# Optimization experiments

Hardware: AMD Instinct MI355X
Metric: run time of the kernel (lower is better)

The kernel has to match this reference:

```python
import jax, jax.numpy as jnp
import numpy as np

NUM_BINS = 64
Z_MIN, Z_MAX = -3.0, 1.0
BIN_SIZE = (Z_MAX - Z_MIN) / NUM_BINS
EPS_MEAN = 1e-5
EPS_BN = 1e-5


def setup_inputs() -> dict:
    key = jax.random.key(0)
    k1, k2, k3, k4 = jax.random.split(key, 4)
    M, N, C = 100000, 64, 4
    feat_channels, out_dim = 64, NUM_BINS * 3
    features = jax.random.normal(k1, (M, N, C), dtype=jnp.float32)
    num_points = jax.random.randint(k2, (M,), 0, 65, dtype=jnp.int32)
    coors = jax.random.randint(k3, (M, 4), 0, 100, dtype=jnp.int32)
    W = jax.random.normal(k4, (feat_channels, out_dim), dtype=jnp.float32) * (1.0 / np.sqrt(out_dim))
    b = jnp.zeros((feat_channels,), dtype=jnp.float32)
    gamma = jnp.ones((feat_channels,), dtype=jnp.float32)
    beta = jnp.zeros((feat_channels,), dtype=jnp.float32)
    return {"features": features, "num_points": num_points, "coors": coors,
            "W": W, "b": b, "gamma": gamma, "beta": beta}


def reference(features, num_points, coors, W, b, gamma, beta):
    M, N, C = features.shape
    # validity mask per point
    mask = (jnp.arange(N)[None, :] < num_points[:, None]).astype(features.dtype)  # [M, N]
    z = features[..., 2]  # [M, N]
    r = features[..., 3]  # [M, N]
    bin_idx = jnp.clip(((z - Z_MIN) / BIN_SIZE).astype(jnp.int32), 0, NUM_BINS - 1)  # [M, N]

    rows = jnp.arange(M)[:, None]  # [M, 1] broadcast against [M, N]
    zeros = jnp.zeros((M, NUM_BINS), dtype=features.dtype)
    count = zeros.at[rows, bin_idx].add(mask)
    sum_z = zeros.at[rows, bin_idx].add(z * mask)
    sum_r = zeros.at[rows, bin_idx].add(r * mask)
    mean_z = sum_z / (count + EPS_MEAN)
    mean_r = sum_r / (count + EPS_MEAN)

    # interleaved layout [count, mean_z, mean_r] per bin -> [M, 3*NUM_BINS]
    hist = jnp.stack([count, mean_z, mean_r], axis=-1).reshape(M, NUM_BINS * 3)

    # Linear -> BatchNorm1d (training: biased batch stats) -> ReLU
    x = hist @ W.T + b  # [M, feat_channels]
    mu = jnp.mean(x, axis=0)
    var = jnp.mean((x - mu) ** 2, axis=0)
    xn = (x - mu) / jnp.sqrt(var + EPS_BN)
    return jax.nn.relu(xn * gamma + beta)
```

## Files before the change

kernel.cpp:

```cpp
#include <hip/hip_runtime.h>
#include <hip/hip_bf16.h>
#include <math.h>


typedef __attribute__((ext_vector_type(8))) short bf16x8;
typedef __attribute__((ext_vector_type(4))) float f32x4;
typedef __attribute__((ext_vector_type(4))) int   i32x4;

#define ZMINF   (-3.0f)
#define INV_BIN 16.0f
#define HROWS   16
#define HPAD    196
#define SZF     524288.0f
#define INV_SZF (1.0f / 524288.0f)
#define TSC     16777216.0f
#define INV_TSC (1.0f / 16777216.0f)
#define REPS    16

__device__ __forceinline__ short f2bf(float f) {
    __hip_bfloat16 h = __float2bfloat16(f);
    return __builtin_bit_cast(short, h);
}

__global__ __launch_bounds__(256)
void k0_prep(const float* __restrict__ W,
             short*       __restrict__ wsW,
             unsigned long long* __restrict__ totals)
{
    const int tid = threadIdx.x;
    for (int e = tid; e < 24 * 64 * 8; e += 256) {
        const int j  = e & 7;
        const int ln = (e >> 3) & 63;
        const int st = e >> 9;
        const int s  = st >> 2, t = st & 3;
        const int k  = s * 32 + (ln >> 4) * 8 + j;
        const int n  = t * 16 + (ln & 15);
        const int wc = (k < 64) ? 3 * k
                     : (k < 128) ? 3 * (k - 64) + 1
                                 : 3 * (k - 128) + 2;
        wsW[e] = f2bf(W[n * 192 + wc]);
    }
    for (int e = tid; e < REPS * 128; e += 256) totals[e] = 0ull;
}

__global__ __launch_bounds__(256, 3)
void k1_hist_mfma(const float4* __restrict__ feat,
                  const int*    __restrict__ nump,
                  const bf16x8* __restrict__ wsWf,
                  const float*  __restrict__ bvec,
                  float*        __restrict__ xout,
                  unsigned long long* __restrict__ totals,
                  int M)
{
    __shared__ int sH[4 * HROWS * HPAD];

    const int tid  = threadIdx.x;
    const int wave = tid >> 6;
    const int lane = tid & 63;
    const int col  = lane & 15;
    const int quad = lane >> 4;

    const int gbase = (blockIdx.x * 4 + wave) * HROWS;
    int* hw = &sH[wave * HROWS * HPAD];
    float psum[4] = {0.f, 0.f, 0.f, 0.f};
    float psq[4]  = {0.f, 0.f, 0.f, 0.f};

    if (gbase < M) {
        i32x4* p4 = (i32x4*)hw;
        #pragma unroll
        for (int i = 0; i < 13; ++i) {
            const int idx = lane + i * 64;
            if (idx < (HROWS * HPAD) / 4) p4[idx] = i32x4{0, 0, 0, 0};
        }
        __builtin_amdgcn_wave_barrier();

        float4 v[HROWS]; int np[HROWS];
        #pragma unroll
        for (int u = 0; u < HROWS; ++u) {
            const int row = gbase + u;
            const int rc  = min(row, M - 1);
            v[u]  = feat[(size_t)rc * 64 + lane];
            np[u] = (row < M) ? nump[rc] : 0;
        }
        #pragma unroll
        for (int u = 0; u < HROWS; ++u) {
            if (lane < np[u]) {
                const float z = v[u].z, rr = v[u].w;
                int bi = (int)((z - ZMINF) * INV_BIN);
                bi = min(max(bi, 0), 63);
                int* hrow = hw + u * HPAD;
                atomicAdd(hrow + bi, 1);
                atomicAdd(hrow + 64 + bi, (int)(z * SZF));
                atomicAdd(hrow + 128 + bi, (int)(rr * SZF));
            }
        }
        __builtin_amdgcn_wave_barrier();
        __threadfence_block();

        f32x4 acc[4] = {};
        bf16x8 bcur[4], bnxt[4];
        #pragma unroll
        for (int t = 0; t < 4; ++t) bcur[t] = wsWf[t * 64 + lane];

        const int* ar = hw + col * HPAD + quad * 8;
        float c0[8], c1[8];
        #pragma unroll
        for (int s = 0; s < 6; ++s) {
            if (s < 5) {
                #pragma unroll
                for (int t = 0; t < 4; ++t) bnxt[t] = wsWf[((s + 1) * 4 + t) * 64 + lane];
            }
            const i32x4* ap = (const i32x4*)(ar + s * 32);
            const i32x4 a0 = ap[0], a1 = ap[1];
            const int iv[8] = {a0.x, a0.y, a0.z, a0.w, a1.x, a1.y, a1.z, a1.w};
            float av[8];
            if (s == 0) {
                #pragma unroll
                for (int j = 0; j < 8; ++j) { c0[j] = (float)iv[j]; av[j] = c0[j]; }
            } else if (s == 1) {
                #pragma unroll
                for (int j = 0; j < 8; ++j) { c1[j] = (float)iv[j]; av[j] = c1[j]; }
            } else if (s == 2) {
                #pragma unroll
                for (int j = 0; j < 8; ++j) {
                    c0[j] = __builtin_amdgcn_rcpf(c0[j] + 1e-5f) * INV_SZF;
                    av[j] = (float)iv[j] * c0[j];
                }
            } else if (s == 3) {
                #pragma unroll
                for (int j = 0; j < 8; ++j) {
                    c1[j] = __builtin_amdgcn_rcpf(c1[j] + 1e-5f) * INV_SZF;
                    av[j] = (float)iv[j] * c1[j];
                }
            } else if (s == 4) {
                #pragma unroll
                for (int j = 0; j < 8; ++j) av[j] = (float)iv[j] * c0[j];
            } else {
                #pragma unroll
                for (int j = 0; j < 8; ++j) av[j] = (float)iv[j] * c1[j];
            }
            bf16x8 af;
            #pragma unroll
            for (int j = 0; j < 8; ++j) af[j] = f2bf(av[j]);
            #pragma unroll
            for (int t = 0; t < 4; ++t)
                acc[t] = __builtin_amdgcn_mfma_f32_16x16x32_bf16(af, bcur[t], acc[t], 0, 0, 0);
            #pragma unroll
            for (int t = 0; t < 4; ++t) bcur[t] = bnxt[t];
        }

        #pragma unroll
        for (int t = 0; t < 4; ++t) {
            const float bias = bvec[t * 16 + col];
            #pragma unroll
            for (int i = 0; i < 4; ++i) {
                const int row = gbase + quad * 4 + i;
                if (row < M) {
                    const float xv = acc[t][i] + bias;
                    xout[(size_t)row * 64 + t * 16 + col] = xv;
                    psum[t] += xv;
                    psq[t]  += xv * xv;
                }
            }
        }
    }

    #pragma unroll
    for (int t = 0; t < 4; ++t) {
        psum[t] += __shfl_xor(psum[t], 16);
        psum[t] += __shfl_xor(psum[t], 32);
        psq[t]  += __shfl_xor(psq[t], 16);
        psq[t]  += __shfl_xor(psq[t], 32);
    }
    __syncthreads();
    float* sF = (float*)sH;
    float* hw2 = sF + wave * HROWS * HPAD;
    if (quad == 0) {
        #pragma unroll
        for (int t = 0; t < 4; ++t) {
            hw2[t * 16 + col]      = psum[t];
            hw2[64 + t * 16 + col] = psq[t];
        }
    }
    __syncthreads();
    if (tid < 128) {
        const float tot = sF[tid] + sF[HROWS * HPAD + tid]
                        + sF[2 * HROWS * HPAD + tid] + sF[3 * HROWS * HPAD + tid];
        unsigned long long* dst = totals + (blockIdx.x & (REPS - 1)) * 128 + tid;
        atomicAdd(dst, (unsigned long long)(long long)(tot * TSC));
    }
}

__global__ __launch_bounds__(256)
void k3_bn_apply(float4* __restrict__ x,
                 const unsigned long long* __restrict__ totals,
                 const float* __restrict__ gamma,
                 const float* __restrict__ beta,
                 float invM, int n4)
{
    __shared__ float sT[128];
    __shared__ float sa[64];
    __shared__ float sc[64];
    const int t = threadIdx.x;
    if (t < 128) {
        long long s = 0;
        #pragma unroll
        for (int rep = 0; rep < REPS; ++rep) s += (long long)totals[rep * 128 + t];
        sT[t] = (float)s * (invM * INV_TSC);
    }
    __syncthreads();
    if (t < 64) {
        const float mu   = sT[t];
        const float q    = sT[64 + t];
        const float var  = q - mu * mu;
        const float rstd = 1.0f / sqrtf(var + 1e-5f);
        const float a    = gamma[t] * rstd;
        sa[t] = a;
        sc[t] = beta[t] - mu * a;
    }
    __syncthreads();
    const int i = blockIdx.x * 256 + t;
    if (i >= n4) return;
    const float4 a = ((const float4*)sa)[i & 15];
    const float4 c = ((const float4*)sc)[i & 15];
    float4 v = x[i];
    v.x = fmaxf(fmaf(v.x, a.x, c.x), 0.f);
    v.y = fmaxf(fmaf(v.y, a.y, c.y), 0.f);
    v.z = fmaxf(fmaf(v.z, a.z, c.z), 0.f);
    v.w = fmaxf(fmaf(v.w, a.w, c.w), 0.f);
    x[i] = v;
}

extern "C" void kernel_launch(void* const* d_in, const int* in_sizes, int n_in,
                              void* d_out, int out_size, void* d_ws, size_t ws_size,
                              hipStream_t stream) {
    const float4* feat  = (const float4*)d_in[0];
    const int*    nump  = (const int*)d_in[1];
    const float*  W     = (const float*)d_in[3];
    const float*  bvec  = (const float*)d_in[4];
    const float*  gamma = (const float*)d_in[5];
    const float*  beta  = (const float*)d_in[6];

    const int M = in_sizes[1];
    float* xout = (float*)d_out;
    short* wsW  = (short*)d_ws;
    unsigned long long* totals =
        (unsigned long long*)((char*)d_ws + 24 * 64 * 8 * sizeof(short));

    k0_prep<<<1, 256, 0, stream>>>(W, wsW, totals);

    const int nblk = (M + 4 * HROWS - 1) / (4 * HROWS);
    k1_hist_mfma<<<nblk, 256, 0, stream>>>(feat, nump, (const bf16x8*)wsW, bvec, xout, totals, M);

    const int n4 = out_size / 4;
    k3_bn_apply<<<(n4 + 255) / 256, 256, 0, stream>>>((float4*)d_out, totals, gamma, beta,
                                                      1.0f / (float)M, n4);
}
```

Measured before the change: 206.1 us.

## Make histogram kernel persistent with prefetching and load only z/r halves

The histogram+MFMA kernel becomes a persistent grid of 512 blocks whose waves loop over row groups, prefetching the next group's features while the current one is processed. Only the z and r components are loaded, as uint2, and the per-row point counts come from one per-lane load followed by readlane. The block-level LDS reduction of BN statistics is replaced by per-wave atomics into 64 replica slots. The BN apply kernel becomes grid-stride with 16 float4 per thread. These trade occupancy-based latency hiding for explicit software prefetch and add more global atomics per block.

Result: slower. 231.6 us (+12.3%).

```diff
diff --git a/kernel.cpp b/kernel.cpp
--- a/kernel.cpp
+++ b/kernel.cpp
@@ -15,7 +15,9 @@
 #define INV_SZF (1.0f / 524288.0f)
 #define TSC     16777216.0f
 #define INV_TSC (1.0f / 16777216.0f)
-#define REPS    16
+#define REPS    64
+#define NBLK1   512
+#define NWAVES  (NBLK1 * 4)
 
 __device__ __forceinline__ short f2bf(float f) {
     __hip_bfloat16 h = __float2bfloat16(f);
@@ -44,13 +46,13 @@
 }
 
 __global__ __launch_bounds__(256, 3)
-void k1_hist_mfma(const float4* __restrict__ feat,
+void k1_hist_mfma(const uint2*  __restrict__ feat2,
                   const int*    __restrict__ nump,
                   const bf16x8* __restrict__ wsWf,
                   const float*  __restrict__ bvec,
                   float*        __restrict__ xout,
                   unsigned long long* __restrict__ totals,
-                  int M)
+                  int M, int G)
 {
     __shared__ int sH[4 * HROWS * HPAD];
 
@@ -59,33 +61,47 @@
     const int lane = tid & 63;
     const int col  = lane & 15;
     const int quad = lane >> 4;
-
-    const int gbase = (blockIdx.x * 4 + wave) * HROWS;
+    const int gw   = blockIdx.x * 4 + wave;
+
     int* hw = &sH[wave * HROWS * HPAD];
     float psum[4] = {0.f, 0.f, 0.f, 0.f};
     float psq[4]  = {0.f, 0.f, 0.f, 0.f};
 
-    if (gbase < M) {
+    uint2 zw[HROWS];
+    int   npv = 0;
+
+    int g = gw;
+    if (g < G) {
+        const int gbase = g * HROWS;
+        #pragma unroll
+        for (int u = 0; u < HROWS; ++u) {
+            const int rc = min(gbase + u, M - 1);
+            zw[u] = feat2[((size_t)rc * 64 + lane) * 2 + 1];
+        }
+        npv = nump[min(gbase + (lane & 15), M - 1)];
+    }
+
+    {
         i32x4* p4 = (i32x4*)hw;
         #pragma unroll
         for (int i = 0; i < 13; ++i) {
             const int idx = lane + i * 64;
             if (idx < (HROWS * HPAD) / 4) p4[idx] = i32x4{0, 0, 0, 0};
         }
-        __builtin_amdgcn_wave_barrier();
-
-        float4 v[HROWS]; int np[HROWS];
+    }
+    __builtin_amdgcn_wave_barrier();
+
+    for (; g < G; g += NWAVES) {
+        const int gbase  = g * HROWS;
+        const int nvalid = min(M - gbase, HROWS);
+
         #pragma unroll
         for (int u = 0; u < HROWS; ++u) {
-            const int row = gbase + u;
-            const int rc  = min(row, M - 1);
-            v[u]  = feat[(size_t)rc * 64 + lane];
-            np[u] = (row < M) ? nump[rc] : 0;
-        }
-        #pragma unroll
-        for (int u = 0; u < HROWS; ++u) {
-            if (lane < np[u]) {
-                const float z = v[u].z, rr = v[u].w;
+            int np_u = __builtin_amdgcn_readlane(npv, u);
+            np_u = (u < nvalid) ? np_u : 0;
+            if (lane < np_u) {
+                const float z  = __int_as_float((int)zw[u].x);
+                const float rr = __int_as_float((int)zw[u].y);
                 int bi = (int)((z - ZMINF) * INV_BIN);
                 bi = min(max(bi, 0), 63);
                 int* hrow = hw + u * HPAD;
@@ -94,6 +110,18 @@
                 atomicAdd(hrow + 128 + bi, (int)(rr * SZF));
             }
         }
+
+        const int gn = g + NWAVES;
+        if (gn < G) {
+            const int nb = gn * HROWS;
+            #pragma unroll
+            for (int u = 0; u < HROWS; ++u) {
+                const int rc = min(nb + u, M - 1);
+                zw[u] = feat2[((size_t)rc * 64 + lane) * 2 + 1];
+            }
+            npv = nump[min(nb + (lane & 15), M - 1)];
+        }
+
         __builtin_amdgcn_wave_barrier();
         __threadfence_block();
 
@@ -163,6 +191,16 @@
                 }
             }
         }
+
+        {
+            i32x4* p4 = (i32x4*)hw;
+            #pragma unroll
+            for (int i = 0; i < 13; ++i) {
+                const int idx = lane + i * 64;
+                if (idx < (HROWS * HPAD) / 4) p4[idx] = i32x4{0, 0, 0, 0};
+            }
+        }
+        __builtin_amdgcn_wave_barrier();
     }
 
     #pragma unroll
@@ -172,23 +210,13 @@
         psq[t]  += __shfl_xor(psq[t], 16);
         psq[t]  += __shfl_xor(psq[t], 32);
     }
-    __syncthreads();
-    float* sF = (float*)sH;
-    float* hw2 = sF + wave * HROWS * HPAD;
-    if (quad == 0) {
-        #pragma unroll
-        for (int t = 0; t < 4; ++t) {
-            hw2[t * 16 + col]      = psum[t];
-            hw2[64 + t * 16 + col] = psq[t];
-        }
-    }
-    __syncthreads();
-    if (tid < 128) {
-        const float tot = sF[tid] + sF[HROWS * HPAD + tid]
-                        + sF[2 * HROWS * HPAD + tid] + sF[3 * HROWS * HPAD + tid];
-        unsigned long long* dst = totals + (blockIdx.x & (REPS - 1)) * 128 + tid;
-        atomicAdd(dst, (unsigned long long)(long long)(tot * TSC));
-    }
+    float myS = psum[0], myQ = psq[0];
+    if (quad == 1) { myS = psum[1]; myQ = psq[1]; }
+    if (quad == 2) { myS = psum[2]; myQ = psq[2]; }
+    if (quad == 3) { myS = psum[3]; myQ = psq[3]; }
+    unsigned long long* dst = totals + (gw & (REPS - 1)) * 128 + lane;
+    atomicAdd(dst,      (unsigned long long)(long long)(myS * TSC));
+    atomicAdd(dst + 64, (unsigned long long)(long long)(myQ * TSC));
 }
 
 __global__ __launch_bounds__(256)
@@ -204,7 +232,7 @@
     const int t = threadIdx.x;
     if (t < 128) {
         long long s = 0;
-        #pragma unroll
+        #pragma unroll 8
         for (int rep = 0; rep < REPS; ++rep) s += (long long)totals[rep * 128 + t];
         sT[t] = (float)s * (invM * INV_TSC);
     }
@@ -219,22 +247,23 @@
         sc[t] = beta[t] - mu * a;
     }
     __syncthreads();
-    const int i = blockIdx.x * 256 + t;
-    if (i >= n4) return;
-    const float4 a = ((const float4*)sa)[i & 15];
-    const float4 c = ((const float4*)sc)[i & 15];
-    float4 v = x[i];
-    v.x = fmaxf(fmaf(v.x, a.x, c.x), 0.f);
-    v.y = fmaxf(fmaf(v.y, a.y, c.y), 0.f);
-    v.z = fmaxf(fmaf(v.z, a.z, c.z), 0.f);
-    v.w = fmaxf(fmaf(v.w, a.w, c.w), 0.f);
-    x[i] = v;
+    const int stride = gridDim.x * 256;
+    for (int i = blockIdx.x * 256 + t; i < n4; i += stride) {
+        const float4 a = ((const float4*)sa)[i & 15];
+        const float4 c = ((const float4*)sc)[i & 15];
+        float4 v = x[i];
+        v.x = fmaxf(fmaf(v.x, a.x, c.x), 0.f);
+        v.y = fmaxf(fmaf(v.y, a.y, c.y), 0.f);
+        v.z = fmaxf(fmaf(v.z, a.z, c.z), 0.f);
+        v.w = fmaxf(fmaf(v.w, a.w, c.w), 0.f);
+        x[i] = v;
+    }
 }
 
 extern "C" void kernel_launch(void* const* d_in, const int* in_sizes, int n_in,
                               void* d_out, int out_size, void* d_ws, size_t ws_size,
                               hipStream_t stream) {
-    const float4* feat  = (const float4*)d_in[0];
+    const uint2*  feat2 = (const uint2*)d_in[0];
     const int*    nump  = (const int*)d_in[1];
     const float*  W     = (const float*)d_in[3];
     const float*  bvec  = (const float*)d_in[4];
@@ -249,10 +278,11 @@
 
     k0_prep<<<1, 256, 0, stream>>>(W, wsW, totals);
 
-    const int nblk = (M + 4 * HROWS - 1) / (4 * HROWS);
-    k1_hist_mfma<<<nblk, 256, 0, stream>>>(feat, nump, (const bf16x8*)wsW, bvec, xout, totals, M);
+    const int G = (M + HROWS - 1) / HROWS;
+    k1_hist_mfma<<<NBLK1, 256, 0, stream>>>(feat2, nump, (const bf16x8*)wsW, bvec, xout, totals, M, G);
 
     const int n4 = out_size / 4;
-    k3_bn_apply<<<(n4 + 255) / 256, 256, 0, stream>>>((float4*)d_out, totals, gamma, beta,
-                                                      1.0f / (float)M, n4);
-}
+    const int nblk3 = (n4 + 256 * 16 - 1) / (256 * 16);
+    k3_bn_apply<<<nblk3, 256, 0, stream>>>((float4*)d_out, totals, gamma, beta,
+                                           1.0f / (float)M, n4);
+}
```
